# Optimization experiments

Measured on AMD Instinct MI355X. Metric: run time of the kernel, lower is better.

Reference implementation:

```python
import jax, jax.numpy as jnp
import numpy as np
import math

B, T, D = 2, 2048, 1024
H = 16
DH = D // H  # 64
ROPE_BASE = 10000.0


def _rope_tables(seq_len, d_head, dtype=jnp.float32):
    inv_freq = 1.0 / (ROPE_BASE ** (jnp.arange(0, d_head, 2, dtype=jnp.float32) / d_head))
    pos = jnp.arange(seq_len, dtype=jnp.float32)
    freqs = jnp.outer(pos, inv_freq)            # [T, DH/2]
    emb = jnp.concatenate([freqs, freqs], -1)   # [T, DH]
    return jnp.cos(emb).astype(dtype), jnp.sin(emb).astype(dtype)


def _rotate_half(x):
    half = x.shape[-1] // 2
    return jnp.concatenate([-x[..., half:], x[..., :half]], axis=-1)


def setup_inputs() -> dict:
    key = jax.random.key(0)
    k1, k2, k3 = jax.random.split(key, 3)
    x = jax.random.normal(k1, (B, T, D), dtype=jnp.float32)
    qkv_w = jax.random.normal(k2, (D, 3 * D), dtype=jnp.float32) * (1.0 / math.sqrt(D))
    out_w = jax.random.normal(k3, (D, D), dtype=jnp.float32) * (1.0 / math.sqrt(D))
    out_b = jnp.zeros((D,), dtype=jnp.float32)
    mask = jnp.tril(jnp.ones((T, T), dtype=bool))[None, None]  # causal [1,1,T,T]
    return {"x": x, "mask": mask, "qkv_w": qkv_w, "out_w": out_w, "out_b": out_b}


def reference(x, mask, qkv_w, out_w, out_b):
    Bv, Tv, Dv = x.shape
    qkv = (x @ qkv_w).reshape(Bv, Tv, 3, H, DH)
    # [B, H, T, DH]
    q = jnp.transpose(qkv[:, :, 0], (0, 2, 1, 3))
    k = jnp.transpose(qkv[:, :, 1], (0, 2, 1, 3))
    v = jnp.transpose(qkv[:, :, 2], (0, 2, 1, 3))
    cos, sin = _rope_tables(Tv, DH, x.dtype)
    cos = cos[None, None]  # [1,1,T,DH]
    sin = sin[None, None]
    q = q * cos + _rotate_half(q) * sin
    k = k * cos + _rotate_half(k) * sin
    scores = jnp.einsum('bhqd,bhkd->bhqk', q, k) / math.sqrt(DH)
    scores = jnp.where(mask, scores, -jnp.inf)
    probs = jax.nn.softmax(scores, axis=-1)  # dropout = identity in eval mode
    out = jnp.einsum('bhqk,bhkd->bhqd', probs, v)
    out = jnp.transpose(out, (0, 2, 1, 3)).reshape(Bv, Tv, Dv)
    return out @ out_w + out_b
```

## Files before the change

### kernel.cpp

```cpp
#include <hip/hip_runtime.h>
#include <math.h>

typedef __attribute__((ext_vector_type(8))) short short8;
typedef __attribute__((ext_vector_type(4))) float f32x4;

static __device__ __forceinline__ unsigned short f2bf(float f) {
  unsigned u = __builtin_bit_cast(unsigned, f);
  u += 0x7fffu + ((u >> 16) & 1u);
  return (unsigned short)(u >> 16);
}
static __device__ __forceinline__ float bf2f(unsigned short h) {
  return __builtin_bit_cast(float, ((unsigned)h) << 16);
}
static __device__ __forceinline__ unsigned pack2bf(float a, float b) {
  return (unsigned)f2bf(a) | ((unsigned)f2bf(b) << 16);
}

typedef __attribute__((address_space(3))) unsigned short lds_us;
typedef __attribute__((address_space(1))) const unsigned short gbl_us;

static __device__ __forceinline__ void gld_lds16(const unsigned short* g,
                                                 unsigned short* l) {
  __builtin_amdgcn_global_load_lds((gbl_us*)g, (lds_us*)l, 16, 0, 0);
}

__global__ __launch_bounds__(256) void cast_x(const float* __restrict__ x,
                                              unsigned short* __restrict__ xb) {
  int i = (blockIdx.x * 256 + threadIdx.x) * 8;
  float4 a = *(const float4*)(x + i);
  float4 b = *(const float4*)(x + i + 4);
  ushort4 u0 = {f2bf(a.x), f2bf(a.y), f2bf(a.z), f2bf(a.w)};
  ushort4 u1 = {f2bf(b.x), f2bf(b.y), f2bf(b.z), f2bf(b.w)};
  *(ushort4*)(xb + i) = u0;
  *(ushort4*)(xb + i + 4) = u1;
}

__global__ __launch_bounds__(256) void tcast(const float* __restrict__ in,
                                             unsigned short* __restrict__ out,
                                             int R, int C) {
  __shared__ unsigned short T[64][68];
  const int r0 = blockIdx.y * 64, c0 = blockIdx.x * 64;
  const int tr = threadIdx.x >> 2;
  const int tc = (threadIdx.x & 3) * 16;
#pragma unroll
  for (int j = 0; j < 4; ++j) {
    float4 v = *(const float4*)(in + (size_t)(r0 + tr) * C + c0 + tc + j * 4);
    ushort4 u = {f2bf(v.x), f2bf(v.y), f2bf(v.z), f2bf(v.w)};
    *(ushort4*)&T[tr][tc + j * 4] = u;
  }
  __syncthreads();
  const int oc = tr;
#pragma unroll
  for (int g = 0; g < 4; ++g) {
    ushort4 u;
    u.x = T[tc + g * 4 + 0][oc];
    u.y = T[tc + g * 4 + 1][oc];
    u.z = T[tc + g * 4 + 2][oc];
    u.w = T[tc + g * 4 + 3][oc];
    *(ushort4*)(out + (size_t)(c0 + oc) * R + r0 + tc + g * 4) = u;
  }
}

template <int MODE>
__global__ __launch_bounds__(256) void gemm_mfma(
    const unsigned short* __restrict__ A, const unsigned short* __restrict__ BT,
    unsigned short* __restrict__ qo, unsigned short* __restrict__ ko,
    unsigned short* __restrict__ vo, const float* __restrict__ bias,
    float* __restrict__ out) {
  __shared__ unsigned short As[4096];
  __shared__ unsigned short Bs[4096];
  const int tid = threadIdx.x;
  const int w = tid >> 6;
  const int lane = tid & 63;
  const int l15 = lane & 15;
  const int quad = lane >> 4;
  const int wm = w >> 1, wn = w & 1;
  const int m0 = blockIdx.y * 128;
  const int n0 = blockIdx.x * 128;

  f32x4 acc[4][4];
  const f32x4 zero4 = {0.f, 0.f, 0.f, 0.f};
#pragma unroll
  for (int mt = 0; mt < 4; ++mt)
#pragma unroll
    for (int nt = 0; nt < 4; ++nt) acc[mt][nt] = zero4;

  int srow[2], skch[2];
#pragma unroll
  for (int i = 0; i < 2; ++i) {
    int c = i * 256 + w * 64 + lane;
    srow[i] = c >> 2;
    skch[i] = (c & 3) ^ ((srow[i] >> 1) & 3);
  }
  const unsigned short* gA[2];
  const unsigned short* gB[2];
#pragma unroll
  for (int i = 0; i < 2; ++i) {
    gA[i] = A + (size_t)(m0 + srow[i]) * 1024 + skch[i] * 8;
    gB[i] = BT + (size_t)(n0 + srow[i]) * 1024 + skch[i] * 8;
  }
  unsigned short* lA[2];
  unsigned short* lB[2];
#pragma unroll
  for (int i = 0; i < 2; ++i) {
    int c = i * 256 + w * 64 + lane;
    lA[i] = As + c * 8;
    lB[i] = Bs + c * 8;
  }

  const int swz = (quad ^ ((l15 >> 1) & 3)) * 8;
  int aoff[4], boff[4];
#pragma unroll
  for (int t = 0; t < 4; ++t) {
    aoff[t] = (wm * 64 + t * 16 + l15) * 32 + swz;
    boff[t] = (wn * 64 + t * 16 + l15) * 32 + swz;
  }

  for (int k0 = 0; k0 < 1024; k0 += 32) {
    __syncthreads();
#pragma unroll
    for (int i = 0; i < 2; ++i) {
      gld_lds16(gA[i] + k0, lA[i]);
      gld_lds16(gB[i] + k0, lB[i]);
    }
    __syncthreads();

    short8 af[4], bf[4];
#pragma unroll
    for (int t = 0; t < 4; ++t) {
      af[t] = *(const short8*)(As + aoff[t]);
      bf[t] = *(const short8*)(Bs + boff[t]);
    }
#pragma unroll
    for (int mt = 0; mt < 4; ++mt)
#pragma unroll
      for (int nt = 0; nt < 4; ++nt)
        acc[mt][nt] =
            __builtin_amdgcn_mfma_f32_16x16x32_bf16(af[mt], bf[nt], acc[mt][nt], 0, 0, 0);
  }

  if constexpr (MODE == 0) {
    const int b = m0 >> 11;
    const int nbase = n0 + wn * 64;
    const int which = nbase >> 10;
    const int h = (nbase & 1023) >> 6;
    const int bh = b * 16 + h;
    if (which < 2) {
      unsigned short* dst = which ? ko : qo;
      const float qs = (which == 0) ? 0.1803368801111f : 1.0f;
      float inv0 = expf(-((float)l15 / 32.f) * 9.21034037198f);
      float inv1 = expf(-((float)(16 + l15) / 32.f) * 9.21034037198f);
#pragma unroll
      for (int mt = 0; mt < 4; ++mt)
#pragma unroll
        for (int r = 0; r < 4; ++r) {
          int t = (m0 + wm * 64 + mt * 16 + quad * 4 + r) & 2047;
          float s0, c0, s1, c1;
          sincosf((float)t * inv0, &s0, &c0);
          sincosf((float)t * inv1, &s1, &c1);
          float x0 = acc[mt][0][r], x1 = acc[mt][1][r];
          float x2 = acc[mt][2][r], x3 = acc[mt][3][r];
          size_t rowoff = ((size_t)bh * 2048 + t) * 64 + l15;
          dst[rowoff + 0]  = f2bf((x0 * c0 - x2 * s0) * qs);
          dst[rowoff + 16] = f2bf((x1 * c1 - x3 * s1) * qs);
          dst[rowoff + 32] = f2bf((x2 * c0 + x0 * s0) * qs);
          dst[rowoff + 48] = f2bf((x3 * c1 + x1 * s1) * qs);
        }
    } else {
#pragma unroll
      for (int mt = 0; mt < 4; ++mt) {
        int t0 = (m0 + wm * 64 + mt * 16 + quad * 4) & 2047;
#pragma unroll
        for (int nt = 0; nt < 4; ++nt) {
          int dh = nt * 16 + l15;
          ushort4 st = {f2bf(acc[mt][nt][0]), f2bf(acc[mt][nt][1]),
                        f2bf(acc[mt][nt][2]), f2bf(acc[mt][nt][3])};
          *(ushort4*)(vo + ((size_t)bh * 64 + dh) * 2048 + t0) = st;
        }
      }
    }
  } else {
    const int nbase = n0 + wn * 64;
    float bv[4];
#pragma unroll
    for (int nt = 0; nt < 4; ++nt) bv[nt] = bias[nbase + nt * 16 + l15];
#pragma unroll
    for (int mt = 0; mt < 4; ++mt)
#pragma unroll
      for (int r = 0; r < 4; ++r) {
        int m = m0 + wm * 64 + mt * 16 + quad * 4 + r;
        float* orow = out + (size_t)m * 1024 + nbase + l15;
#pragma unroll
        for (int nt = 0; nt < 4; ++nt) orow[nt * 16] = acc[mt][nt][r] + bv[nt];
      }
  }
}

__device__ __constant__ unsigned char SLOT_QB[48] = {
    16, 17, 18, 19, 20, 21, 22, 23, 24, 25, 26, 27, 28, 29, 30, 31,
    15, 31, 14, 30, 13, 29, 12, 28, 11, 27, 10, 26, 9,  25, 8,  24,
    7,  23, 6,  22, 5,  21, 4,  20, 3,  19, 2,  18, 1,  17, 0,  16};
__device__ __constant__ unsigned char SLOT_CH[48] = {
    0, 0, 0, 0, 0, 0, 0, 0, 0, 0, 0, 0, 0, 0, 0, 0,
    0, 1, 0, 1, 0, 1, 0, 1, 0, 1, 0, 1, 0, 1, 0, 1,
    0, 1, 0, 1, 0, 1, 0, 1, 0, 1, 0, 1, 0, 1, 0, 1};

__global__ __launch_bounds__(256) void attn_mfma(
    const unsigned short* __restrict__ qg, const unsigned short* __restrict__ kg,
    const unsigned short* __restrict__ vtg, unsigned short* __restrict__ og,
    unsigned short* __restrict__ Opart, float* __restrict__ Lpart) {
  constexpr int LDP = 72;
  __shared__ unsigned short Ks[2][4096];
  __shared__ unsigned short Vt[2][4096];
  __shared__ unsigned short Ps[4 * 16 * LDP];
  const int bh = blockIdx.y;
  const int slot = blockIdx.x;
  const int qb = SLOT_QB[slot];
  const int chunk = SLOT_CH[slot];
  const int kb0 = chunk ? 16 : 0;
  const int kbn = chunk ? (qb + 1) : min(qb + 1, 16);
  const int tid = threadIdx.x;
  const int w = tid >> 6;
  const int lane = tid & 63;
  const int l15 = lane & 15;
  const int quad = lane >> 4;

  const int gq0 = qb * 64;
  const int qw = w * 16;

  const unsigned short* qrow = qg + ((size_t)bh * 2048 + gq0 + qw + l15) * 64;
  short8 qf0 = *(const short8*)(qrow + quad * 8);
  short8 qf1 = *(const short8*)(qrow + quad * 8 + 32);

  f32x4 acc_o[4];
  const f32x4 zero4 = {0.f, 0.f, 0.f, 0.f};
#pragma unroll
  for (int nt = 0; nt < 4; ++nt) acc_o[nt] = zero4;
  float lsum = 0.f;

  const unsigned short* kbase = kg + (size_t)bh * 2048 * 64;
  const unsigned short* vtbase = vtg + (size_t)bh * 64 * 2048;
  unsigned short* pb = &Ps[w * 16 * LDP];
  const int prow = l15 * LDP;

  auto issue = [&](int kb, int buf) {
    const unsigned short* ksrc = kbase + (size_t)(kb * 64) * 64;
    const unsigned short* vsrc = vtbase + kb * 64;
#pragma unroll
    for (int i = 0; i < 2; ++i) {
      int c = (w * 2 + i) * 64 + lane;
      int row = c >> 3, d = c & 7;
      int sc = d ^ (row & 7);
      gld_lds16(ksrc + row * 64 + sc * 8, &Ks[buf][c * 8]);
      gld_lds16(vsrc + (size_t)row * 2048 + sc * 8, &Vt[buf][c * 8]);
    }
  };

  const int kc0 = (quad ^ (l15 & 7)) * 8;
  const int kc1 = kc0 ^ 32;

  issue(kb0, 0);
  for (int kb = kb0; kb < kbn; ++kb) {
    const int cur = (kb - kb0) & 1;
    __syncthreads();
    if (kb + 1 < kbn) issue(kb + 1, cur ^ 1);

    const unsigned short* kt = Ks[cur];
    const unsigned short* vt = Vt[cur];

    f32x4 s[4];
#pragma unroll
    for (int nt = 0; nt < 4; ++nt) {
      const unsigned short* kr = kt + (nt * 16 + l15) * 64;
      short8 kf0 = *(const short8*)(kr + kc0);
      short8 kf1 = *(const short8*)(kr + kc1);
      f32x4 c = zero4;
      c = __builtin_amdgcn_mfma_f32_16x16x32_bf16(kf0, qf0, c, 0, 0, 0);
      c = __builtin_amdgcn_mfma_f32_16x16x32_bf16(kf1, qf1, c, 0, 0, 0);
      s[nt] = c;
    }

    if (kb == qb) {
#pragma unroll
      for (int nt = 0; nt < 4; ++nt) {
        int klocal = nt * 16 + quad * 4;
        int qlocal = qw + l15;
#pragma unroll
        for (int r = 0; r < 4; ++r)
          if (klocal + r > qlocal) s[nt][r] = -INFINITY;
      }
    }

#pragma unroll
    for (int nt = 0; nt < 4; ++nt) {
      float e0 = exp2f(s[nt][0]);
      float e1 = exp2f(s[nt][1]);
      float e2 = exp2f(s[nt][2]);
      float e3 = exp2f(s[nt][3]);
      lsum += (e0 + e1) + (e2 + e3);
      int col = nt * 16 + quad * 4;
      *(unsigned*)&pb[prow + col] = pack2bf(e0, e1);
      *(unsigned*)&pb[prow + col + 2] = pack2bf(e2, e3);
    }

    short8 pf0 = *(const short8*)&pb[prow + quad * 8];
    short8 pf1 = *(const short8*)&pb[prow + 32 + quad * 8];

#pragma unroll
    for (int nt = 0; nt < 4; ++nt) {
      const unsigned short* vr = vt + (nt * 16 + l15) * 64;
      short8 vf0 = *(const short8*)(vr + kc0);
      short8 vf1 = *(const short8*)(vr + kc1);
      acc_o[nt] = __builtin_amdgcn_mfma_f32_16x16x32_bf16(vf0, pf0, acc_o[nt], 0, 0, 0);
      acc_o[nt] = __builtin_amdgcn_mfma_f32_16x16x32_bf16(vf1, pf1, acc_o[nt], 0, 0, 0);
    }
  }

  lsum += __shfl_xor(lsum, 16);
  lsum += __shfl_xor(lsum, 32);

  if (qb < 16) {
    float inv_l = 1.0f / lsum;
    const int b = bh >> 4;
    const int h = bh & 15;
    unsigned short* orow =
        og + ((size_t)(b * 2048 + gq0 + qw + l15)) * 1024 + h * 64 + quad * 4;
#pragma unroll
    for (int nt = 0; nt < 4; ++nt) {
      *(unsigned*)(orow + nt * 16) =
          pack2bf(acc_o[nt][0] * inv_l, acc_o[nt][1] * inv_l);
      *(unsigned*)(orow + nt * 16 + 2) =
          pack2bf(acc_o[nt][2] * inv_l, acc_o[nt][3] * inv_l);
    }
  } else {
    const int p = (bh * 16 + (qb - 16)) * 2 + chunk;
    unsigned short* orow = Opart + (size_t)p * 4096 + (qw + l15) * 64 + quad * 4;
#pragma unroll
    for (int nt = 0; nt < 4; ++nt) {
      *(unsigned*)(orow + nt * 16) = pack2bf(acc_o[nt][0], acc_o[nt][1]);
      *(unsigned*)(orow + nt * 16 + 2) = pack2bf(acc_o[nt][2], acc_o[nt][3]);
    }
    if (quad == 0) Lpart[p * 64 + qw + l15] = lsum;
  }
}

__global__ __launch_bounds__(256) void attn_combine(
    const unsigned short* __restrict__ Opart, const float* __restrict__ Lpart,
    unsigned short* __restrict__ og) {
  int i = blockIdx.x * 256 + threadIdx.x;
  int dh = (i & 15) * 4;
  int q = (i >> 4) & 63;
  int qb16 = (i >> 10) & 15;
  int bh = i >> 14;
  int p0 = (bh * 16 + qb16) * 2;
  ushort4 a = *(const ushort4*)(Opart + (size_t)p0 * 4096 + q * 64 + dh);
  ushort4 b = *(const ushort4*)(Opart + (size_t)(p0 + 1) * 4096 + q * 64 + dh);
  float inv = 1.0f / (Lpart[p0 * 64 + q] + Lpart[(p0 + 1) * 64 + q]);
  float o0 = (bf2f(a.x) + bf2f(b.x)) * inv;
  float o1 = (bf2f(a.y) + bf2f(b.y)) * inv;
  float o2 = (bf2f(a.z) + bf2f(b.z)) * inv;
  float o3 = (bf2f(a.w) + bf2f(b.w)) * inv;
  int bb = bh >> 4, h = bh & 15;
  int t = 1024 + qb16 * 64 + q;
  unsigned short* orow = og + ((size_t)(bb * 2048 + t)) * 1024 + h * 64 + dh;
  *(unsigned*)(orow) = pack2bf(o0, o1);
  *(unsigned*)(orow + 2) = pack2bf(o2, o3);
}

extern "C" void kernel_launch(void* const* d_in, const int* in_sizes, int n_in,
                              void* d_out, int out_size, void* d_ws,
                              size_t ws_size, hipStream_t stream) {
  const float* x = (const float*)d_in[0];
  const float* qkv_w = (const float*)d_in[2];
  const float* out_w = (const float*)d_in[3];
  const float* out_b = (const float*)d_in[4];
  float* out = (float*)d_out;

  unsigned short* xb = (unsigned short*)d_ws;
  unsigned short* wqkvT = xb + 4194304;
  unsigned short* woT = wqkvT + 3145728;
  unsigned short* qb16 = woT + 1048576;
  unsigned short* kb16 = qb16 + 4194304;
  unsigned short* vt16 = kb16 + 4194304;
  unsigned short* ab = vt16 + 4194304;
  unsigned short* Opart = ab + 4194304;
  float* Lpart = (float*)(Opart + 4194304);

  cast_x<<<2048, 256, 0, stream>>>(x, xb);
  tcast<<<dim3(48, 16), 256, 0, stream>>>(qkv_w, wqkvT, 1024, 3072);
  tcast<<<dim3(16, 16), 256, 0, stream>>>(out_w, woT, 1024, 1024);
  gemm_mfma<0><<<dim3(24, 32), 256, 0, stream>>>(xb, wqkvT, qb16, kb16, vt16,
                                                 nullptr, nullptr);
  attn_mfma<<<dim3(48, 32), 256, 0, stream>>>(qb16, kb16, vt16, ab, Opart,
                                              Lpart);
  attn_combine<<<2048, 256, 0, stream>>>(Opart, Lpart, ab);
  gemm_mfma<1><<<dim3(8, 32), 256, 0, stream>>>(ab, woT, nullptr, nullptr,
                                                nullptr, out_b, out);
}
```

Measured before the change: 227.3 us.

## Split causal attention KV range into up to four chunks per query block

Replaces the two-way split for late query blocks with a graded split (1 to 4 chunks depending on query block index), launching 80 slots per head instead of 48 so the work per block is more uniform. The combine kernel now sums a variable number of partials, and the extra partial buffer reuses the x bf16 workspace region. P tile in LDS switches to an XOR-swizzled 64-wide layout and a truncating perm-based bf16 pack. This risks more partial-write and combine traffic, and the truncated rounding changes precision slightly.

```diff
diff --git a/kernel.cpp b/kernel.cpp
--- a/kernel.cpp
+++ b/kernel.cpp
@@ -14,6 +14,10 @@
 }
 static __device__ __forceinline__ unsigned pack2bf(float a, float b) {
   return (unsigned)f2bf(a) | ((unsigned)f2bf(b) << 16);
+}
+static __device__ __forceinline__ unsigned pack2bf_t(float a, float b) {
+  return __builtin_amdgcn_perm(__builtin_bit_cast(unsigned, b),
+                               __builtin_bit_cast(unsigned, a), 0x07060302u);
 }
 
 typedef __attribute__((address_space(3))) unsigned short lds_us;
@@ -196,29 +200,37 @@
   }
 }
 
-__device__ __constant__ unsigned char SLOT_QB[48] = {
-    16, 17, 18, 19, 20, 21, 22, 23, 24, 25, 26, 27, 28, 29, 30, 31,
-    15, 31, 14, 30, 13, 29, 12, 28, 11, 27, 10, 26, 9,  25, 8,  24,
-    7,  23, 6,  22, 5,  21, 4,  20, 3,  19, 2,  18, 1,  17, 0,  16};
-__device__ __constant__ unsigned char SLOT_CH[48] = {
-    0, 0, 0, 0, 0, 0, 0, 0, 0, 0, 0, 0, 0, 0, 0, 0,
-    0, 1, 0, 1, 0, 1, 0, 1, 0, 1, 0, 1, 0, 1, 0, 1,
-    0, 1, 0, 1, 0, 1, 0, 1, 0, 1, 0, 1, 0, 1, 0, 1};
-
 __global__ __launch_bounds__(256) void attn_mfma(
     const unsigned short* __restrict__ qg, const unsigned short* __restrict__ kg,
     const unsigned short* __restrict__ vtg, unsigned short* __restrict__ og,
-    unsigned short* __restrict__ Opart, float* __restrict__ Lpart) {
-  constexpr int LDP = 72;
+    unsigned short* __restrict__ OpA,
+    unsigned short* __restrict__ OpB,
+    float* __restrict__ Lpart) {
   __shared__ unsigned short Ks[2][4096];
   __shared__ unsigned short Vt[2][4096];
-  __shared__ unsigned short Ps[4 * 16 * LDP];
+  __shared__ unsigned short Ps[4 * 16 * 64];
   const int bh = blockIdx.y;
   const int slot = blockIdx.x;
-  const int qb = SLOT_QB[slot];
-  const int chunk = SLOT_CH[slot];
-  const int kb0 = chunk ? 16 : 0;
-  const int kbn = chunk ? (qb + 1) : min(qb + 1, 16);
+  int qb, chunk;
+  if (slot < 32) {
+    qb = 24 + (slot & 7);
+    chunk = slot >> 3;
+  } else if (slot < 56) {
+    int s = slot - 32;
+    qb = 16 + (s & 7);
+    chunk = s >> 3;
+  } else if (slot < 72) {
+    int s = slot - 56;
+    qb = 8 + (s & 7);
+    chunk = s >> 3;
+  } else {
+    qb = slot - 72;
+    chunk = 0;
+  }
+  const int n = qb >= 24 ? 4 : (qb >= 16 ? 3 : (qb >= 8 ? 2 : 1));
+  const int t0 = chunk * (qb + 1) / n;
+  const int t1 = (chunk + 1) * (qb + 1) / n;
+
   const int tid = threadIdx.x;
   const int w = tid >> 6;
   const int lane = tid & 63;
@@ -240,8 +252,9 @@
 
   const unsigned short* kbase = kg + (size_t)bh * 2048 * 64;
   const unsigned short* vtbase = vtg + (size_t)bh * 64 * 2048;
-  unsigned short* pb = &Ps[w * 16 * LDP];
-  const int prow = l15 * LDP;
+  unsigned short* pb = &Ps[w * 16 * 64];
+  const int prow = l15 * 64;
+  const int psw = l15 & 7;
 
   auto issue = [&](int kb, int buf) {
     const unsigned short* ksrc = kbase + (size_t)(kb * 64) * 64;
@@ -256,14 +269,14 @@
     }
   };
 
-  const int kc0 = (quad ^ (l15 & 7)) * 8;
+  const int kc0 = (quad ^ psw) * 8;
   const int kc1 = kc0 ^ 32;
 
-  issue(kb0, 0);
-  for (int kb = kb0; kb < kbn; ++kb) {
-    const int cur = (kb - kb0) & 1;
+  issue(t0, 0);
+  for (int kb = t0; kb < t1; ++kb) {
+    const int cur = (kb - t0) & 1;
     __syncthreads();
-    if (kb + 1 < kbn) issue(kb + 1, cur ^ 1);
+    if (kb + 1 < t1) issue(kb + 1, cur ^ 1);
 
     const unsigned short* kt = Ks[cur];
     const unsigned short* vt = Vt[cur];
@@ -298,13 +311,13 @@
       float e2 = exp2f(s[nt][2]);
       float e3 = exp2f(s[nt][3]);
       lsum += (e0 + e1) + (e2 + e3);
-      int col = nt * 16 + quad * 4;
-      *(unsigned*)&pb[prow + col] = pack2bf(e0, e1);
-      *(unsigned*)&pb[prow + col + 2] = pack2bf(e2, e3);
-    }
-
-    short8 pf0 = *(const short8*)&pb[prow + quad * 8];
-    short8 pf1 = *(const short8*)&pb[prow + 32 + quad * 8];
+      int base = prow + ((nt * 2 + (quad >> 1)) ^ psw) * 8 + (quad & 1) * 4;
+      *(unsigned*)&pb[base] = pack2bf_t(e0, e1);
+      *(unsigned*)&pb[base + 2] = pack2bf_t(e2, e3);
+    }
+
+    short8 pf0 = *(const short8*)&pb[prow + (quad ^ psw) * 8];
+    short8 pf1 = *(const short8*)&pb[prow + ((4 + quad) ^ psw) * 8];
 
 #pragma unroll
     for (int nt = 0; nt < 4; ++nt) {
@@ -319,7 +332,7 @@
   lsum += __shfl_xor(lsum, 16);
   lsum += __shfl_xor(lsum, 32);
 
-  if (qb < 16) {
+  if (n == 1) {
     float inv_l = 1.0f / lsum;
     const int b = bh >> 4;
     const int h = bh & 15;
@@ -333,38 +346,53 @@
           pack2bf(acc_o[nt][2] * inv_l, acc_o[nt][3] * inv_l);
     }
   } else {
-    const int p = (bh * 16 + (qb - 16)) * 2 + chunk;
-    unsigned short* orow = Opart + (size_t)p * 4096 + (qw + l15) * 64 + quad * 4;
+    const int pidx = (qb < 16) ? (qb - 8) * 2 + chunk
+                               : (qb < 24) ? 16 + (qb - 16) * 3 + chunk
+                                           : 40 + (qb - 24) * 4 + chunk;
+    unsigned short* obase = (pidx < 16)
+                                ? OpB + ((size_t)(bh * 16 + pidx)) * 4096
+                                : OpA + ((size_t)(bh * 56 + (pidx - 16))) * 4096;
+    unsigned short* orow = obase + (qw + l15) * 64 + quad * 4;
 #pragma unroll
     for (int nt = 0; nt < 4; ++nt) {
       *(unsigned*)(orow + nt * 16) = pack2bf(acc_o[nt][0], acc_o[nt][1]);
       *(unsigned*)(orow + nt * 16 + 2) = pack2bf(acc_o[nt][2], acc_o[nt][3]);
     }
-    if (quad == 0) Lpart[p * 64 + qw + l15] = lsum;
+    if (quad == 0) Lpart[(bh * 72 + pidx) * 64 + qw + l15] = lsum;
   }
 }
 
 __global__ __launch_bounds__(256) void attn_combine(
-    const unsigned short* __restrict__ Opart, const float* __restrict__ Lpart,
-    unsigned short* __restrict__ og) {
+    const unsigned short* __restrict__ OpA, const unsigned short* __restrict__ OpB,
+    const float* __restrict__ Lpart, unsigned short* __restrict__ og) {
   int i = blockIdx.x * 256 + threadIdx.x;
   int dh = (i & 15) * 4;
   int q = (i >> 4) & 63;
-  int qb16 = (i >> 10) & 15;
-  int bh = i >> 14;
-  int p0 = (bh * 16 + qb16) * 2;
-  ushort4 a = *(const ushort4*)(Opart + (size_t)p0 * 4096 + q * 64 + dh);
-  ushort4 b = *(const ushort4*)(Opart + (size_t)(p0 + 1) * 4096 + q * 64 + dh);
-  float inv = 1.0f / (Lpart[p0 * 64 + q] + Lpart[(p0 + 1) * 64 + q]);
-  float o0 = (bf2f(a.x) + bf2f(b.x)) * inv;
-  float o1 = (bf2f(a.y) + bf2f(b.y)) * inv;
-  float o2 = (bf2f(a.z) + bf2f(b.z)) * inv;
-  float o3 = (bf2f(a.w) + bf2f(b.w)) * inv;
+  int idx = i >> 10;
+  int bh = idx / 24;
+  int qr = idx - bh * 24;
+  int qb = 8 + qr;
+  int count = qr < 8 ? 2 : (qr < 16 ? 3 : 4);
+  int pstart = qr < 8 ? qr * 2 : (qr < 16 ? 16 + (qr - 8) * 3 : 40 + (qr - 16) * 4);
+  float o0 = 0.f, o1 = 0.f, o2 = 0.f, o3 = 0.f, l = 0.f;
+  for (int c = 0; c < count; ++c) {
+    int pidx = pstart + c;
+    const unsigned short* obase =
+        (pidx < 16) ? OpB + ((size_t)(bh * 16 + pidx)) * 4096
+                    : OpA + ((size_t)(bh * 56 + (pidx - 16))) * 4096;
+    ushort4 a = *(const ushort4*)(obase + q * 64 + dh);
+    o0 += bf2f(a.x);
+    o1 += bf2f(a.y);
+    o2 += bf2f(a.z);
+    o3 += bf2f(a.w);
+    l += Lpart[(bh * 72 + pidx) * 64 + q];
+  }
+  float inv = 1.0f / l;
   int bb = bh >> 4, h = bh & 15;
-  int t = 1024 + qb16 * 64 + q;
+  int t = qb * 64 + q;
   unsigned short* orow = og + ((size_t)(bb * 2048 + t)) * 1024 + h * 64 + dh;
-  *(unsigned*)(orow) = pack2bf(o0, o1);
-  *(unsigned*)(orow + 2) = pack2bf(o2, o3);
+  *(unsigned*)(orow) = pack2bf(o0 * inv, o1 * inv);
+  *(unsigned*)(orow + 2) = pack2bf(o2 * inv, o3 * inv);
 }
 
 extern "C" void kernel_launch(void* const* d_in, const int* in_sizes, int n_in,
@@ -383,17 +411,18 @@
   unsigned short* kb16 = qb16 + 4194304;
   unsigned short* vt16 = kb16 + 4194304;
   unsigned short* ab = vt16 + 4194304;
-  unsigned short* Opart = ab + 4194304;
-  float* Lpart = (float*)(Opart + 4194304);
+  unsigned short* OpB = ab + 4194304;
+  float* Lpart = (float*)(OpB + 4194304);
+  unsigned short* OpA = xb;
 
   cast_x<<<2048, 256, 0, stream>>>(x, xb);
   tcast<<<dim3(48, 16), 256, 0, stream>>>(qkv_w, wqkvT, 1024, 3072);
   tcast<<<dim3(16, 16), 256, 0, stream>>>(out_w, woT, 1024, 1024);
   gemm_mfma<0><<<dim3(24, 32), 256, 0, stream>>>(xb, wqkvT, qb16, kb16, vt16,
                                                  nullptr, nullptr);
-  attn_mfma<<<dim3(48, 32), 256, 0, stream>>>(qb16, kb16, vt16, ab, Opart,
+  attn_mfma<<<dim3(80, 32), 256, 0, stream>>>(qb16, kb16, vt16, ab, OpA, OpB,
                                               Lpart);
-  attn_combine<<<2048, 256, 0, stream>>>(Opart, Lpart, ab);
+  attn_combine<<<3072, 256, 0, stream>>>(OpA, OpB, Lpart, ab);
   gemm_mfma<1><<<dim3(8, 32), 256, 0, stream>>>(ab, woT, nullptr, nullptr,
                                                 nullptr, out_b, out);
 }
```

New measurement: 217.6 us. -4.3%, faster.
